# Performance work log

Hardware: AMD Instinct MI355X
Metric: run time of the kernel (lower is better)

## Reference

```python
import jax, jax.numpy as jnp
import numpy as np
from jax import lax

TOPK = 10
THRESHOLD = 0.5
MARGIN = 0.5
EPS = 1e-8


def setup_inputs() -> dict:
    key = jax.random.key(0)
    k1, k2 = jax.random.split(key)
    B, C, H, W = 8, 256, 128, 128
    loc_features = jax.random.normal(k1, (B, C, H, W), dtype=jnp.float32)
    det_features = jax.random.normal(k2, (B, C, H, W), dtype=jnp.float32)
    return {"loc_features": loc_features, "det_features": det_features}


def _peak_features(fmap):
    """fmap: [C,H,W] -> (feats [TOPK,C], valid [TOPK] bool).
    Peaks = pixels equal to their 3x3 local max with intensity > THRESHOLD,
    sorted by intensity descending, top TOPK (padded with invalid slots)."""
    C, H, W = fmap.shape
    intensity = jnp.sqrt(jnp.sum(fmap * fmap, axis=0))  # [H,W] L2 norm over channels
    pooled = lax.reduce_window(intensity, -jnp.inf, lax.max,
                               (3, 3), (1, 1), 'SAME')
    peak_mask = (intensity == pooled) & (intensity > THRESHOLD)
    masked = jnp.where(peak_mask, intensity, -jnp.inf).reshape(-1)  # [H*W]
    vals, idx = lax.top_k(masked, TOPK)
    valid = jnp.isfinite(vals)  # slots beyond the actual peak count are -inf
    y = idx // W
    x = idx % W
    feats = fmap[:, y, x].T  # [TOPK, C]
    return feats, valid


def _cosine_sim(a, b):
    # a: [Ka,C], b: [Kb,C]; torch.cosine_similarity semantics with eps clamp
    na = jnp.maximum(jnp.linalg.norm(a, axis=-1), EPS)  # [Ka]
    nb = jnp.maximum(jnp.linalg.norm(b, axis=-1), EPS)  # [Kb]
    return (a @ b.T) / (na[:, None] * nb[None, :])


def _per_sample_loss(det_map, loc_map):
    det_f, det_v = _peak_features(det_map)
    loc_f, loc_v = _peak_features(loc_map)
    sim = _cosine_sim(det_f, loc_f)  # [TOPK, TOPK]
    pair_mask = det_v[:, None] & loc_v[None, :]
    n_pairs = jnp.sum(pair_mask)
    loss_sum = jnp.sum(jnp.where(pair_mask, jax.nn.relu(sim - MARGIN), 0.0))
    # torch 'continue' when either side has no peaks -> contributes 0
    return jnp.where(n_pairs > 0, loss_sum / jnp.maximum(n_pairs, 1).astype(sim.dtype), 0.0)


def reference(loc_features, det_features):
    B = loc_features.shape[0]
    losses = jax.vmap(_per_sample_loss)(det_features, loc_features)  # [B]
    return jnp.sum(losses) / B
```

## Files before the change

### kernel.cpp

```cpp
#include <hip/hip_runtime.h>
#include <math.h>

namespace {
constexpr int kB = 8;
constexpr int kC = 256;
constexpr int kH = 128;
constexpr int kW = 128;
constexpr int kHW = kH * kW;
constexpr int kTopK = 10;
constexpr float kThreshold = 0.5f;
constexpr float kMargin = 0.5f;
constexpr float kEps = 1e-8f;
constexpr int kMaps = 2 * kB;
constexpr int kChunks = 4;
constexpr int kCPer = kC / kChunks;
}

__global__ __launch_bounds__(256) void partial_kernel(
    const float* __restrict__ loc, const float* __restrict__ det,
    float* __restrict__ partial) {
  const int bid = blockIdx.x;
  const int m = bid >> 6;
  const int r = bid & 63;
  const int chunk = r >> 4;
  const int g = (r & 15) * 256 + threadIdx.x;
  const int p = g * 4;
  const float* __restrict__ src = (m < kB) ? loc : det;
  const int b = m & (kB - 1);
  const float* base =
      src + (size_t)b * kC * kHW + (size_t)(chunk * kCPer) * kHW + p;
  float ax = 0.f, ay = 0.f, az = 0.f, aw = 0.f;
  for (int c0 = 0; c0 < kCPer; c0 += 8) {
    float4 v[8];
#pragma unroll
    for (int u = 0; u < 8; ++u)
      v[u] = *(const float4*)(base + (size_t)(c0 + u) * kHW);
#pragma unroll
    for (int u = 0; u < 8; ++u) {
      ax = fmaf(v[u].x, v[u].x, ax);
      ay = fmaf(v[u].y, v[u].y, ay);
      az = fmaf(v[u].z, v[u].z, az);
      aw = fmaf(v[u].w, v[u].w, aw);
    }
  }
  float4 o = {ax, ay, az, aw};
  *(float4*)(partial + (size_t)chunk * kMaps * kHW + (size_t)m * kHW + p) = o;
}

__global__ __launch_bounds__(1024) void topk_kernel(
    const float* __restrict__ partial, float* __restrict__ inten,
    float* __restrict__ tvals, int* __restrict__ tidx) {
  const int m = blockIdx.x;
  const int t = threadIdx.x;
  float* __restrict__ I = inten + (size_t)m * kHW;

#pragma unroll
  for (int k = 0; k < 4; ++k) {
    const int p = (k * 1024 + t) * 4;
    const float* pp = partial + (size_t)m * kHW + p;
    float4 s = *(const float4*)(pp);
#pragma unroll
    for (int ch = 1; ch < kChunks; ++ch) {
      const float4 q = *(const float4*)(pp + (size_t)ch * kMaps * kHW);
      s.x += q.x; s.y += q.y; s.z += q.z; s.w += q.w;
    }
    float4 o = {sqrtf(s.x), sqrtf(s.y), sqrtf(s.z), sqrtf(s.w)};
    *(float4*)(I + p) = o;
  }
  __syncthreads();

  float v[16];
#pragma unroll
  for (int k = 0; k < 16; ++k) {
    const int p = k * 1024 + t;
    const int y = p >> 7;
    const int x = p & (kW - 1);
    const float c0 = I[p];
    float nmax = -INFINITY;
    for (int dy = -1; dy <= 1; ++dy) {
      const int yy = y + dy;
      if (yy < 0 || yy >= kH) continue;
      for (int dx = -1; dx <= 1; ++dx) {
        const int xx = x + dx;
        if (xx < 0 || xx >= kW) continue;
        nmax = fmaxf(nmax, I[yy * kW + xx]);
      }
    }
    const bool peak = (c0 > kThreshold) && (c0 >= nmax);
    v[k] = peak ? c0 : -INFINITY;
  }

  __shared__ float s_wv[16];
  __shared__ int s_wi[16];
  __shared__ int s_bi;
  const int wave = t >> 6;
  const int lane = t & 63;

  for (int r = 0; r < kTopK; ++r) {
    float bv = v[0];
    int bi = t;
#pragma unroll
    for (int k = 1; k < 16; ++k) {
      const int idx = k * 1024 + t;
      if (v[k] > bv || (v[k] == bv && idx < bi)) { bv = v[k]; bi = idx; }
    }
    for (int off = 32; off > 0; off >>= 1) {
      const float ov = __shfl_down(bv, off, 64);
      const int oi = __shfl_down(bi, off, 64);
      if (ov > bv || (ov == bv && oi < bi)) { bv = ov; bi = oi; }
    }
    if (lane == 0) { s_wv[wave] = bv; s_wi[wave] = bi; }
    __syncthreads();
    if (t == 0) {
      float xv = s_wv[0];
      int xi = s_wi[0];
      for (int w2 = 1; w2 < 16; ++w2) {
        if (s_wv[w2] > xv || (s_wv[w2] == xv && s_wi[w2] < xi)) {
          xv = s_wv[w2];
          xi = s_wi[w2];
        }
      }
      s_bi = xi;
      tvals[m * kTopK + r] = xv;
      tidx[m * kTopK + r] = xi;
    }
    __syncthreads();
    const int wi = s_bi;
    if ((wi & 1023) == t) v[wi >> 10] = -INFINITY;
    __syncthreads();
  }
}

__global__ __launch_bounds__(256) void loss_kernel(
    const float* __restrict__ loc, const float* __restrict__ det,
    const float* __restrict__ tvals, const int* __restrict__ tidx,
    float* __restrict__ losses) {
  const int b = blockIdx.x;
  const int t = threadIdx.x;
  __shared__ float ds[kTopK][kC + 1];
  __shared__ float ls[kTopK][kC + 1];
  __shared__ float s_red[kC];

  float lv[kTopK], dv[kTopK];
  int li[kTopK], di[kTopK];
#pragma unroll
  for (int i = 0; i < kTopK; ++i) {
    lv[i] = tvals[b * kTopK + i];
    li[i] = tidx[b * kTopK + i];
    dv[i] = tvals[(kB + b) * kTopK + i];
    di[i] = tidx[(kB + b) * kTopK + i];
  }
  const float* lb = loc + (size_t)b * kC * kHW + (size_t)t * kHW;
  const float* db = det + (size_t)b * kC * kHW + (size_t)t * kHW;
#pragma unroll
  for (int i = 0; i < kTopK; ++i) {
    ls[i][t] = lb[li[i]];
    ds[i][t] = db[di[i]];
  }
  __syncthreads();

  float contrib = 0.f;
  if (t < kTopK * kTopK) {
    const int i = t / kTopK;
    const int j = t % kTopK;
    const bool valid = (dv[i] > -1e30f) && (lv[j] > -1e30f);
    if (valid) {
      float dot = 0.f;
#pragma unroll 8
      for (int c = 0; c < kC; ++c) dot = fmaf(ds[i][c], ls[j][c], dot);
      const float na = fmaxf(dv[i], kEps);
      const float nb = fmaxf(lv[j], kEps);
      const float sim = dot / (na * nb);
      contrib = fmaxf(sim - kMargin, 0.f);
    }
  }
  s_red[t] = contrib;
  __syncthreads();
  if (t == 0) {
    int nd = 0, nl = 0;
    for (int i = 0; i < kTopK; ++i) {
      nd += (dv[i] > -1e30f) ? 1 : 0;
      nl += (lv[i] > -1e30f) ? 1 : 0;
    }
    float s = 0.f;
    for (int k = 0; k < kTopK * kTopK; ++k) s += s_red[k];
    const int np = nd * nl;
    losses[b] = (np > 0) ? (s / (float)np) : 0.f;
  }
}

__global__ void final_kernel(const float* __restrict__ losses,
                             float* __restrict__ out) {
  if (threadIdx.x == 0 && blockIdx.x == 0) {
    float s = 0.f;
    for (int i = 0; i < kB; ++i) s += losses[i];
    out[0] = s / (float)kB;
  }
}

extern "C" void kernel_launch(void* const* d_in, const int* in_sizes, int n_in,
                              void* d_out, int out_size, void* d_ws,
                              size_t ws_size, hipStream_t stream) {
  const float* loc = (const float*)d_in[0];
  const float* det = (const float*)d_in[1];
  float* out = (float*)d_out;

  float* wsf = (float*)d_ws;
  float* partial = wsf;
  float* inten = partial + (size_t)kChunks * kMaps * kHW;
  float* tvals = inten + (size_t)kMaps * kHW;
  int* tidx = (int*)(tvals + kMaps * kTopK);
  float* losses = (float*)(tidx + kMaps * kTopK);

  partial_kernel<<<dim3(kMaps * kChunks * 16), dim3(256), 0, stream>>>(
      loc, det, partial);
  topk_kernel<<<dim3(kMaps), dim3(1024), 0, stream>>>(partial, inten, tvals,
                                                      tidx);
  loss_kernel<<<dim3(kB), dim3(kC), 0, stream>>>(loc, det, tvals, tidx,
                                                 losses);
  final_kernel<<<dim3(1), dim3(64), 0, stream>>>(losses, out);
}
```

Before: 376.5 us.

## Stream channel reduction through LDS with double-buffered async global_load_lds

Rewrites the sum-of-squares pass so each block stages 8 channels at a time into LDS with asynchronous global_load_lds and double-buffers the stages so the next load overlaps the current accumulation. The channel split drops from four chunks to two halves, which halves the block count and the partial buffer the top-k kernel must combine. This aims to keep more loads in flight on a purely bandwidth-bound pass. In exchange it uses 64KB of LDS per block, which limits occupancy, and adds a barrier per stage.

```diff
diff --git a/kernel.cpp b/kernel.cpp
--- a/kernel.cpp
+++ b/kernel.cpp
@@ -12,39 +12,55 @@
 constexpr float kMargin = 0.5f;
 constexpr float kEps = 1e-8f;
 constexpr int kMaps = 2 * kB;
-constexpr int kChunks = 4;
-constexpr int kCPer = kC / kChunks;
-}
-
-__global__ __launch_bounds__(256) void partial_kernel(
+constexpr int kHalves = 2;
+constexpr int kTiles = 16;
+constexpr int kStages = 16;
+}
+
+__global__ __launch_bounds__(256) void sumsq_kernel(
     const float* __restrict__ loc, const float* __restrict__ det,
     float* __restrict__ partial) {
+  __shared__ float lds[2][8 * 1024];
   const int bid = blockIdx.x;
-  const int m = bid >> 6;
-  const int r = bid & 63;
-  const int chunk = r >> 4;
-  const int g = (r & 15) * 256 + threadIdx.x;
-  const int p = g * 4;
+  const int m = bid >> 5;
+  const int h = (bid >> 4) & 1;
+  const int tile = bid & 15;
+  const int t = threadIdx.x;
+  const int w = t >> 6;
+  const int lane = t & 63;
   const float* __restrict__ src = (m < kB) ? loc : det;
   const int b = m & (kB - 1);
-  const float* base =
-      src + (size_t)b * kC * kHW + (size_t)(chunk * kCPer) * kHW + p;
-  float ax = 0.f, ay = 0.f, az = 0.f, aw = 0.f;
-  for (int c0 = 0; c0 < kCPer; c0 += 8) {
-    float4 v[8];
-#pragma unroll
-    for (int u = 0; u < 8; ++u)
-      v[u] = *(const float4*)(base + (size_t)(c0 + u) * kHW);
-#pragma unroll
-    for (int u = 0; u < 8; ++u) {
-      ax = fmaf(v[u].x, v[u].x, ax);
-      ay = fmaf(v[u].y, v[u].y, ay);
-      az = fmaf(v[u].z, v[u].z, az);
-      aw = fmaf(v[u].w, v[u].w, aw);
-    }
-  }
-  float4 o = {ax, ay, az, aw};
-  *(float4*)(partial + (size_t)chunk * kMaps * kHW + (size_t)m * kHW + p) = o;
+  const float* gmap = src + (size_t)b * kC * kHW + (size_t)(h * 128) * kHW +
+                      tile * 1024 + w * 256 + lane * 4;
+
+  auto issue = [&](int s, int buf) {
+    const float* g = gmap + (size_t)(s * 8) * kHW;
+    float* l = &lds[buf][w * 256];
+#pragma unroll
+    for (int j = 0; j < 8; ++j) {
+      __builtin_amdgcn_global_load_lds(
+          (const __attribute__((address_space(1))) void*)(g + (size_t)j * kHW),
+          (__attribute__((address_space(3))) void*)(l + j * 1024), 16, 0, 0);
+    }
+  };
+
+  float4 acc = {0.f, 0.f, 0.f, 0.f};
+  issue(0, 0);
+  for (int s = 0; s < kStages; ++s) {
+    __syncthreads();
+    if (s < kStages - 1) issue(s + 1, (s + 1) & 1);
+    const float* lb = &lds[s & 1][t * 4];
+#pragma unroll
+    for (int j = 0; j < 8; ++j) {
+      const float4 v = *(const float4*)(lb + j * 1024);
+      acc.x = fmaf(v.x, v.x, acc.x);
+      acc.y = fmaf(v.y, v.y, acc.y);
+      acc.z = fmaf(v.z, v.z, acc.z);
+      acc.w = fmaf(v.w, v.w, acc.w);
+    }
+  }
+  *(float4*)(partial + ((size_t)h * kMaps + m) * kHW + tile * 1024 + t * 4) =
+      acc;
 }
 
 __global__ __launch_bounds__(1024) void topk_kernel(
@@ -58,13 +74,10 @@
   for (int k = 0; k < 4; ++k) {
     const int p = (k * 1024 + t) * 4;
     const float* pp = partial + (size_t)m * kHW + p;
-    float4 s = *(const float4*)(pp);
-#pragma unroll
-    for (int ch = 1; ch < kChunks; ++ch) {
-      const float4 q = *(const float4*)(pp + (size_t)ch * kMaps * kHW);
-      s.x += q.x; s.y += q.y; s.z += q.z; s.w += q.w;
-    }
-    float4 o = {sqrtf(s.x), sqrtf(s.y), sqrtf(s.z), sqrtf(s.w)};
+    const float4 a = *(const float4*)(pp);
+    const float4 q = *(const float4*)(pp + (size_t)kMaps * kHW);
+    float4 o = {sqrtf(a.x + q.x), sqrtf(a.y + q.y), sqrtf(a.z + q.z),
+                sqrtf(a.w + q.w)};
     *(float4*)(I + p) = o;
   }
   __syncthreads();
@@ -207,12 +220,12 @@
 
   float* wsf = (float*)d_ws;
   float* partial = wsf;
-  float* inten = partial + (size_t)kChunks * kMaps * kHW;
+  float* inten = partial + (size_t)kHalves * kMaps * kHW;
   float* tvals = inten + (size_t)kMaps * kHW;
   int* tidx = (int*)(tvals + kMaps * kTopK);
   float* losses = (float*)(tidx + kMaps * kTopK);
 
-  partial_kernel<<<dim3(kMaps * kChunks * 16), dim3(256), 0, stream>>>(
+  sumsq_kernel<<<dim3(kMaps * kHalves * kTiles), dim3(256), 0, stream>>>(
       loc, det, partial);
   topk_kernel<<<dim3(kMaps), dim3(1024), 0, stream>>>(partial, inten, tvals,
                                                       tidx);
```

Measured after the change: 377.1 us. Within noise of the previous version (+0.2%).

## Split channel reduction finer and move partial combine into separate parallel kernel

Applied to the files above, without the earlier changes.

The channel sum-of-squares pass now splits channels into 8 chunks instead of 4, doubling the block count to 2048, and adds an occupancy hint in the launch bounds. The combine-and-sqrt step moves out of the 16-block top-k kernel into its own widely parallel kernel, so the serial top-k blocks no longer read all partial buffers. In exchange the partial buffer doubles in size, adding memory traffic, and there is one more kernel launch.

```diff
diff --git a/kernel.cpp b/kernel.cpp
--- a/kernel.cpp
+++ b/kernel.cpp
@@ -12,62 +12,65 @@
 constexpr float kMargin = 0.5f;
 constexpr float kEps = 1e-8f;
 constexpr int kMaps = 2 * kB;
-constexpr int kChunks = 4;
+constexpr int kChunks = 8;
 constexpr int kCPer = kC / kChunks;
-}
-
-__global__ __launch_bounds__(256) void partial_kernel(
+constexpr int kSegs = 16;
+constexpr int kSegPx = kHW / kSegs;
+}
+
+__global__ __launch_bounds__(256, 8) void sumsq_kernel(
     const float* __restrict__ loc, const float* __restrict__ det,
     float* __restrict__ partial) {
   const int bid = blockIdx.x;
-  const int m = bid >> 6;
-  const int r = bid & 63;
-  const int chunk = r >> 4;
-  const int g = (r & 15) * 256 + threadIdx.x;
-  const int p = g * 4;
+  const int m = bid >> 7;
+  const int r = bid & 127;
+  const int ch = r >> 4;
+  const int seg = r & 15;
+  const int t = threadIdx.x;
   const float* __restrict__ src = (m < kB) ? loc : det;
   const int b = m & (kB - 1);
-  const float* base =
-      src + (size_t)b * kC * kHW + (size_t)(chunk * kCPer) * kHW + p;
-  float ax = 0.f, ay = 0.f, az = 0.f, aw = 0.f;
+  const float* base = src + (size_t)b * kC * kHW +
+                      (size_t)(ch * kCPer) * kHW + seg * kSegPx + t * 4;
+  float4 acc = {0.f, 0.f, 0.f, 0.f};
   for (int c0 = 0; c0 < kCPer; c0 += 8) {
     float4 v[8];
 #pragma unroll
-    for (int u = 0; u < 8; ++u)
-      v[u] = *(const float4*)(base + (size_t)(c0 + u) * kHW);
-#pragma unroll
-    for (int u = 0; u < 8; ++u) {
-      ax = fmaf(v[u].x, v[u].x, ax);
-      ay = fmaf(v[u].y, v[u].y, ay);
-      az = fmaf(v[u].z, v[u].z, az);
-      aw = fmaf(v[u].w, v[u].w, aw);
-    }
-  }
-  float4 o = {ax, ay, az, aw};
-  *(float4*)(partial + (size_t)chunk * kMaps * kHW + (size_t)m * kHW + p) = o;
+    for (int j = 0; j < 8; ++j)
+      v[j] = *(const float4*)(base + (size_t)(c0 + j) * kHW);
+#pragma unroll
+    for (int j = 0; j < 8; ++j) {
+      acc.x = fmaf(v[j].x, v[j].x, acc.x);
+      acc.y = fmaf(v[j].y, v[j].y, acc.y);
+      acc.z = fmaf(v[j].z, v[j].z, acc.z);
+      acc.w = fmaf(v[j].w, v[j].w, acc.w);
+    }
+  }
+  *(float4*)(partial + ((size_t)ch * kMaps + m) * kHW + seg * kSegPx +
+             t * 4) = acc;
+}
+
+__global__ __launch_bounds__(256) void combine_kernel(
+    const float* __restrict__ partial, float* __restrict__ inten) {
+  const int g = blockIdx.x * 256 + threadIdx.x;
+  const int m = g >> 12;
+  const int p = (g & 4095) * 4;
+  const float* pp = partial + (size_t)m * kHW + p;
+  float4 s = *(const float4*)(pp);
+#pragma unroll
+  for (int ch = 1; ch < kChunks; ++ch) {
+    const float4 q = *(const float4*)(pp + (size_t)ch * kMaps * kHW);
+    s.x += q.x; s.y += q.y; s.z += q.z; s.w += q.w;
+  }
+  float4 o = {sqrtf(s.x), sqrtf(s.y), sqrtf(s.z), sqrtf(s.w)};
+  *(float4*)(inten + (size_t)m * kHW + p) = o;
 }
 
 __global__ __launch_bounds__(1024) void topk_kernel(
-    const float* __restrict__ partial, float* __restrict__ inten,
-    float* __restrict__ tvals, int* __restrict__ tidx) {
+    const float* __restrict__ inten, float* __restrict__ tvals,
+    int* __restrict__ tidx) {
   const int m = blockIdx.x;
   const int t = threadIdx.x;
-  float* __restrict__ I = inten + (size_t)m * kHW;
-
-#pragma unroll
-  for (int k = 0; k < 4; ++k) {
-    const int p = (k * 1024 + t) * 4;
-    const float* pp = partial + (size_t)m * kHW + p;
-    float4 s = *(const float4*)(pp);
-#pragma unroll
-    for (int ch = 1; ch < kChunks; ++ch) {
-      const float4 q = *(const float4*)(pp + (size_t)ch * kMaps * kHW);
-      s.x += q.x; s.y += q.y; s.z += q.z; s.w += q.w;
-    }
-    float4 o = {sqrtf(s.x), sqrtf(s.y), sqrtf(s.z), sqrtf(s.w)};
-    *(float4*)(I + p) = o;
-  }
-  __syncthreads();
+  const float* __restrict__ I = inten + (size_t)m * kHW;
 
   float v[16];
 #pragma unroll
@@ -212,10 +215,11 @@
   int* tidx = (int*)(tvals + kMaps * kTopK);
   float* losses = (float*)(tidx + kMaps * kTopK);
 
-  partial_kernel<<<dim3(kMaps * kChunks * 16), dim3(256), 0, stream>>>(
+  sumsq_kernel<<<dim3(kMaps * kChunks * kSegs), dim3(256), 0, stream>>>(
       loc, det, partial);
-  topk_kernel<<<dim3(kMaps), dim3(1024), 0, stream>>>(partial, inten, tvals,
-                                                      tidx);
+  combine_kernel<<<dim3(kMaps * kHW / 4 / 256), dim3(256), 0, stream>>>(
+      partial, inten);
+  topk_kernel<<<dim3(kMaps), dim3(1024), 0, stream>>>(inten, tvals, tidx);
   loss_kernel<<<dim3(kB), dim3(kC), 0, stream>>>(loc, det, tvals, tidx,
                                                  losses);
   final_kernel<<<dim3(1), dim3(64), 0, stream>>>(losses, out);
```

Result: faster. 357.4 us (-5.1%).
